# Optimization experiments

Measured on AMD Instinct MI355X. Metric: run time of the kernel, lower is better.

Reference implementation:

```python
import jax, jax.numpy as jnp
import numpy as np

# param tuples: (vdecay, vth, grad_win(=threshold_adaptation), grad_amp, rate_scale)
HID = (0.5, 0.3, 0.3, 1.0, 1.0)
OUT = (0.5, 0.3, 0.3, 1.0, 1.0)

B, I, H, O, T = 128, 1024, 4096, 512, 100


def setup_inputs() -> dict:
    key = jax.random.key(0)
    k1, k2, k3 = jax.random.split(key, 3)
    return {
        "spike_data": jax.random.uniform(k1, (B, I, T), dtype=jnp.float32),
        "hid_spike0": jnp.zeros((B, H), jnp.float32),
        "hid_volt0": jnp.zeros((B, H), jnp.float32),
        "out_spike0": jnp.zeros((B, O), jnp.float32),
        "out_volt0": jnp.zeros((B, O), jnp.float32),
        "w_hid": jax.random.normal(k2, (H, I), dtype=jnp.float32) * 0.02,
        "w_out": jax.random.normal(k3, (O, H), dtype=jnp.float32) * 0.02,
        "batch_size": B,
        "spike_ts": T,
    }


def _spike(volt, p):
    vdecay, vth, grad_win, grad_amp, rate_scale = p
    scaled = rate_scale * volt
    dyn_vth = vth * jnp.tanh(grad_win * jnp.max(scaled))
    return (scaled > dyn_vth).astype(volt.dtype)


def reference(spike_data, hid_spike0, hid_volt0, out_spike0, out_volt0,
              w_hid, w_out, batch_size, spike_ts):
    x = jnp.transpose(spike_data.reshape(batch_size, I, spike_ts), (2, 0, 1))  # [T,B,I]

    def step(carry, xt):
        hs, hv, osp, ov = carry
        hv_new = hv * HID[0] * (1.0 - hs) + xt @ w_hid.T          # [B,H]
        hs_new = _spike(hv_new, HID)
        ov_new = ov * OUT[0] * (1.0 - osp) + hs_new @ w_out.T     # [B,O]
        os_new = _spike(ov_new, OUT)
        return (hs_new, hv_new, os_new, ov_new), os_new

    _, outs = jax.lax.scan(step, (hid_spike0, hid_volt0, out_spike0, out_volt0), x)
    return jnp.sum(outs, axis=0)  # [B,O]
```

## Files before the change

### kernel.cpp

```cpp
#include <hip/hip_runtime.h>
#include <math.h>
#include <stdint.h>

#define T_STEPS 100
#define B_DIM 128
#define I_DIM 1024
#define H_DIM 4096
#define O_DIM 512
#define T_CHUNK 20
#define HS_RING 21
#define HS_SLOT ((size_t)8*128*512)
#define OV_LAG 21
#define RING_S 40
#define TAIL_START 80
#define LEADER 255

typedef _Float16 f16x8 __attribute__((ext_vector_type(8)));
typedef _Float16 f16x4 __attribute__((ext_vector_type(4)));
typedef float    f32x4 __attribute__((ext_vector_type(4)));

#define AS1 __attribute__((address_space(1)))
#define AS3 __attribute__((address_space(3)))

#define ALOAD(p)    __hip_atomic_load((p), __ATOMIC_RELAXED, __HIP_MEMORY_SCOPE_AGENT)
#define ASTORE(p,v) __hip_atomic_store((p), (v), __ATOMIC_RELAXED, __HIP_MEMORY_SCOPE_AGENT)

__device__ __forceinline__ void gload_lds16(const _Float16* g, _Float16* l){
  __builtin_amdgcn_global_load_lds(
      (const AS1 unsigned*)(uintptr_t)g,
      (AS3 unsigned*)(unsigned)(uintptr_t)l, 16, 0, 0);
}

__device__ __forceinline__ unsigned fmap(float f){
  unsigned u = __float_as_uint(f);
  return (u & 0x80000000u) ? ~u : (u | 0x80000000u);
}
__device__ __forceinline__ float funmap(unsigned m){
  unsigned u = (m & 0x80000000u) ? (m & 0x7FFFFFFFu) : ~m;
  return __uint_as_float(u);
}
__device__ __forceinline__ float vth_of(unsigned m){
  return 0.3f * tanhf(0.3f * funmap(m));
}

__global__ __launch_bounds__(256) void init_kernel(float* hv, float* ovs,
                                                   uint32_t* cnt32,
                                                   unsigned* hmaxA, unsigned* omaxA,
                                                   unsigned* hflag, unsigned* oflag)
{
  int i = blockIdx.x * 256 + threadIdx.x;
  if (i < B_DIM*H_DIM) hv[i] = 0.f;
  if (i < B_DIM*O_DIM) ovs[i] = 0.f;
  if (i < B_DIM*O_DIM/4) cnt32[i] = 0u;
  if (i < 100*256) hflag[i] = 0u;
  if (i < 101*32)  oflag[i] = 0u;
  if (i < 128){
    unsigned v = (i==0) ? 0x80000000u : 0u;
    hmaxA[i] = v; omaxA[i] = v;
  }
}

__global__ __launch_bounds__(256) void prep_x(const float* __restrict__ sp,
                                              _Float16* __restrict__ Ahi,
                                              _Float16* __restrict__ Alo, int t0)
{
  __shared__ float tile[32][16][10];
  const int b16 = blockIdx.x, kc = blockIdx.y, tz = blockIdx.z;
  for (int e = threadIdx.x; e < 5120; e += 256){
    int tt = e % 10, row = e / 10;
    int bb = row >> 5, ii = row & 31;
    tile[ii][bb][tt] =
      sp[((size_t)(b16*16+bb)*I_DIM + kc*32 + ii)*T_STEPS + t0 + tz*10 + tt];
  }
  __syncthreads();
  for (int u = threadIdx.x; u < 640; u += 256){
    int tl = u >> 6, l = u & 63, kg = l >> 4, r = l & 15;
    f16x8 hi, lo;
    #pragma unroll
    for (int e=0;e<8;e++){
      float x = tile[kg*8+e][r][tl] * 2048.f;
      _Float16 h = (_Float16)x;
      hi[e] = h;
      lo[e] = (_Float16)(x - (float)h);
    }
    int t_local = tz*10 + tl;
    size_t off = ((size_t)(t_local*8 + b16)*32 + kc)*512 + kg*128 + r*8;
    *(f16x8*)(Ahi + off) = hi;
    *(f16x8*)(Alo + off) = lo;
  }
}

__global__ __launch_bounds__(256) void prep_weights(
    const float* __restrict__ Wh, const float* __restrict__ Wo,
    _Float16* __restrict__ WHhi, _Float16* __restrict__ WHlo,
    _Float16* __restrict__ WOhi, _Float16* __restrict__ WOlo)
{
  const int blk = blockIdx.x;
  if (blk < 256){
    const int n16 = blk;
    for (int u = threadIdx.x; u < 2048; u += 256){
      int kc = u >> 6, l = u & 63, kg = l >> 4, r = l & 15;
      const float* src = Wh + (size_t)(n16*16 + r)*I_DIM + kc*32 + kg*8;
      f16x8 hi, lo;
      #pragma unroll
      for (int e=0;e<8;e++){
        float x = src[e] * 256.f;
        _Float16 h = (_Float16)x;
        hi[e] = h; lo[e] = (_Float16)(x - (float)h);
      }
      size_t off = ((size_t)n16*32 + kc)*512 + kg*128 + r*8;
      *(f16x8*)(WHhi + off) = hi;
      *(f16x8*)(WHlo + off) = lo;
    }
  } else {
    const int n16 = blk - 256;
    for (int u = threadIdx.x; u < 8192; u += 256){
      int kc = u >> 6, l = u & 63, kg = l >> 4, r = l & 15;
      const float* src = Wo + (size_t)(n16*16 + r)*H_DIM + kc*32 + kg*8;
      f16x8 hi, lo;
      #pragma unroll
      for (int e=0;e<8;e++){
        float x = src[e] * 256.f;
        _Float16 h = (_Float16)x;
        hi[e] = h; lo[e] = (_Float16)(x - (float)h);
      }
      size_t off = ((size_t)(n16*128 + kc))*512 + kg*128 + r*8;
      *(f16x8*)(WOhi + off) = hi;
      *(f16x8*)(WOlo + off) = lo;
    }
  }
}

__global__ __launch_bounds__(256, 2) void gemm1_mfma(
    const _Float16* __restrict__ Ahi, const _Float16* __restrict__ Alo,
    const _Float16* __restrict__ Bhi, const _Float16* __restrict__ Blo,
    float* __restrict__ G)
{
  __shared__ __align__(16) _Float16 lds[2][4][8][512];
  const int tid = threadIdx.x, wave = tid>>6, lane = tid&63;
  const int bn = blockIdx.x, bm = blockIdx.y;
  const int wm = wave>>1, wn = wave&1;

  const _Float16* srcbase = (wave==0)?Ahi:(wave==1)?Alo:(wave==2)?Bhi:Blo;
  const int r16b = ((wave<2) ? bm : bn)*8;
  const _Float16* gsrc = srcbase + (size_t)r16b*32*512 + lane*8;

  f32x4 acc[16];
  #pragma unroll
  for (int i=0;i<16;i++) acc[i] = (f32x4){0.f,0.f,0.f,0.f};

  #pragma unroll
  for (int q=0;q<8;q++)
    gload_lds16(gsrc + (size_t)q*32*512, &lds[0][wave][q][0]);

  for (int kc=0;kc<32;kc++){
    __syncthreads();
    if (kc < 31){
      #pragma unroll
      for (int q=0;q<8;q++)
        gload_lds16(gsrc + ((size_t)q*32 + kc+1)*512, &lds[(kc+1)&1][wave][q][0]);
    }
    const int cb = kc&1;
    f16x8 fAh[4], fAl[4], fBh[4], fBl[4];
    #pragma unroll
    for (int i=0;i<4;i++){
      fAh[i] = *(const f16x8*)&lds[cb][0][wm*4+i][lane*8];
      fAl[i] = *(const f16x8*)&lds[cb][1][wm*4+i][lane*8];
      fBh[i] = *(const f16x8*)&lds[cb][2][wn*4+i][lane*8];
      fBl[i] = *(const f16x8*)&lds[cb][3][wn*4+i][lane*8];
    }
    #pragma unroll
    for (int i=0;i<4;i++)
      #pragma unroll
      for (int j=0;j<4;j++)
        acc[i*4+j] = __builtin_amdgcn_mfma_f32_16x16x32_f16(fAh[i], fBh[j], acc[i*4+j], 0,0,0);
    #pragma unroll
    for (int i=0;i<4;i++)
      #pragma unroll
      for (int j=0;j<4;j++)
        acc[i*4+j] = __builtin_amdgcn_mfma_f32_16x16x32_f16(fAh[i], fBl[j], acc[i*4+j], 0,0,0);
    #pragma unroll
    for (int i=0;i<4;i++)
      #pragma unroll
      for (int j=0;j<4;j++)
        acc[i*4+j] = __builtin_amdgcn_mfma_f32_16x16x32_f16(fAl[i], fBh[j], acc[i*4+j], 0,0,0);
  }
  const int colw = lane&15, quad = lane>>4;
  const float sc = 1.f/(2048.f*256.f);
  float* eds = (float*)lds + wave*2048;
  __syncthreads();
  #pragma unroll
  for (int ih=0; ih<2; ih++){
    #pragma unroll
    for (int il=0; il<2; il++){
      int i = ih*2+il;
      #pragma unroll
      for (int j=0;j<4;j++)
        #pragma unroll
        for (int r=0;r<4;r++)
          eds[(il*16 + quad*4 + r)*64 + j*16 + colw] = acc[i*4+j][r]*sc;
    }
    #pragma unroll
    for (int rr8=0; rr8<8; rr8++){
      int row = rr8*4 + quad;
      float4 v = *(float4*)&eds[row*64 + colw*4];
      int m = bm*128 + wm*64 + ih*32 + row;
      int n = bn*128 + wn*64 + colw*4;
      *(float4*)&G[(size_t)m*H_DIM + n] = v;
    }
  }
}

__global__ __launch_bounds__(256) void hv_step(
    const float* __restrict__ Gs, float* __restrict__ hv,
    _Float16* __restrict__ hs_slot,
    const unsigned* __restrict__ hmax_t, unsigned* __restrict__ hmax_n, int t,
    const float* __restrict__ OGp, float* __restrict__ ovs,
    uchar4* __restrict__ cnt8, unsigned* __restrict__ omaxA, int ovt)
{
  __shared__ float red[4];
  const int tid = threadIdx.x, lane = tid&63, wv = tid>>6;

  if (blockIdx.x < 512){
    if (t > T_STEPS) return;
    const int gid = blockIdx.x*256 + tid;
    const int b = gid >> 10, h0 = (gid & 1023) << 2;
    const float vth = vth_of(*hmax_t);
    float4 h = *(const float4*)(hv + (size_t)gid*4);

    if (t > 0){
      const int kc = h0>>5, kg=(h0>>3)&3, e=h0&7, r=b&15, m16l=b>>4;
      f16x4 s;
      s[0]=(h.x>vth)?(_Float16)1:(_Float16)0; s[1]=(h.y>vth)?(_Float16)1:(_Float16)0;
      s[2]=(h.z>vth)?(_Float16)1:(_Float16)0; s[3]=(h.w>vth)?(_Float16)1:(_Float16)0;
      *(f16x4*)(hs_slot + ((size_t)m16l*128 + kc)*512 + kg*128 + r*8 + e) = s;
    }
    if (t < T_STEPS){
      float4 g = *(const float4*)(Gs + (size_t)gid*4);
      float4 o;
      o.x = (h.x>vth ? 0.f : 0.5f*h.x) + g.x;
      o.y = (h.y>vth ? 0.f : 0.5f*h.y) + g.y;
      o.z = (h.z>vth ? 0.f : 0.5f*h.z) + g.z;
      o.w = (h.w>vth ? 0.f : 0.5f*h.w) + g.w;
      *(float4*)(hv + (size_t)gid*4) = o;
      float lmax = fmaxf(fmaxf(o.x,o.y),fmaxf(o.z,o.w));
      #pragma unroll
      for (int off=32; off>0; off>>=1) lmax = fmaxf(lmax, __shfl_down(lmax, off));
      if (lane==0) red[wv] = lmax;
      __syncthreads();
      if (tid==0){
        float m = fmaxf(fmaxf(red[0],red[1]),fmaxf(red[2],red[3]));
        atomicMax(hmax_n, fmap(m));
      }
    }
  } else {
    if (ovt < 0 || ovt >= TAIL_START) return;
    const int f = (int)(blockIdx.x - 512)*256 + tid;
    const float vthp = vth_of(omaxA[ovt]);
    const int slot = ovt % RING_S;
    float lmax = -3.0e38f;
    #pragma unroll
    for (int q=0;q<4;q++){
      int o4 = f + q*4096;
      float4 v = *(const float4*)(ovs + (size_t)o4*4);
      uchar4 c = cnt8[o4];
      bool s0 = v.x > vthp, s1 = v.y > vthp, s2 = v.z > vthp, s3 = v.w > vthp;
      c.x += s0; c.y += s1; c.z += s2; c.w += s3;
      v.x = s0 ? 0.f : 0.5f*v.x;
      v.y = s1 ? 0.f : 0.5f*v.y;
      v.z = s2 ? 0.f : 0.5f*v.z;
      v.w = s3 ? 0.f : 0.5f*v.w;
      float4 g0 = *(const float4*)(OGp + ((size_t)slot*4+0)*(B_DIM*O_DIM) + (size_t)o4*4);
      float4 g1 = *(const float4*)(OGp + ((size_t)slot*4+1)*(B_DIM*O_DIM) + (size_t)o4*4);
      float4 g2 = *(const float4*)(OGp + ((size_t)slot*4+2)*(B_DIM*O_DIM) + (size_t)o4*4);
      float4 g3 = *(const float4*)(OGp + ((size_t)slot*4+3)*(B_DIM*O_DIM) + (size_t)o4*4);
      v.x += (g0.x+g1.x)+(g2.x+g3.x);
      v.y += (g0.y+g1.y)+(g2.y+g3.y);
      v.z += (g0.z+g1.z)+(g2.z+g3.z);
      v.w += (g0.w+g1.w)+(g2.w+g3.w);
      lmax = fmaxf(lmax, fmaxf(fmaxf(v.x,v.y),fmaxf(v.z,v.w)));
      *(float4*)(ovs + (size_t)o4*4) = v;
      cnt8[o4] = c;
    }
    #pragma unroll
    for (int off=32; off>0; off>>=1) lmax = fmaxf(lmax, __shfl_down(lmax, off));
    if (lane==0) red[wv] = lmax;
    __syncthreads();
    if (tid==0){
      float m = fmaxf(fmaxf(red[0],red[1]),fmaxf(red[2],red[3]));
      atomicMax(&omaxA[ovt+1], fmap(m));
    }
  }
}

__global__ __launch_bounds__(512) void hv_chunk(
    const float* __restrict__ Gs,
    float* __restrict__ hv,
    _Float16* __restrict__ HS,
    unsigned* __restrict__ hmaxA,
    const float* __restrict__ OGp, float* __restrict__ ovs,
    uchar4* __restrict__ cnt8, unsigned* __restrict__ omaxA,
    unsigned* __restrict__ hflag, unsigned* __restrict__ oflag,
    int t0, int nsteps)
{
  __shared__ float red[8], redo[8];
  __shared__ unsigned sredH[4];
  __shared__ unsigned sh_h, sh_o;
  const int tid = threadIdx.x, lane = tid&63, wv = tid>>6;
  const int blk = blockIdx.x;
  const int gid = blk*512 + tid;
  const int b = gid >> 10, h0 = (gid & 1023) << 2;
  const int kc = h0>>5, kg=(h0>>3)&3, e=h0&7, r=b&15, m16l=b>>4;
  const bool ovblk = blk < 32;

  float4 h = *(const float4*)(hv + (size_t)gid*4);
  float4 vo = make_float4(0.f,0.f,0.f,0.f);
  unsigned cw = 0;
  if (ovblk){
    vo = *(const float4*)(ovs + (size_t)gid*4);
    uchar4 c0 = cnt8[gid];
    cw = (unsigned)c0.x | ((unsigned)c0.y<<8) | ((unsigned)c0.z<<16) | ((unsigned)c0.w<<24);
  }
  float4 g = *(const float4*)(Gs + (size_t)gid*4);
  unsigned hm_cur = hmaxA[t0];
  unsigned om_cur = 0;
  { int ovt0 = t0 - OV_LAG;
    if (ovblk && ovt0 >= 0 && ovt0 < TAIL_START) om_cur = omaxA[ovt0]; }

  for (int j = 0; j < nsteps; j++){
    const int t = t0 + j;
    const int ovt = t - OV_LAG;
    const bool last = (j == nsteps-1);

    float4 gn = make_float4(0.f,0.f,0.f,0.f);
    if (!last && (t+1) < T_STEPS)
      gn = *(const float4*)(Gs + (size_t)(j+1)*(B_DIM*H_DIM) + (size_t)gid*4);

    const float vth = vth_of(hm_cur);
    {
      f16x4 s;
      s[0]=(h.x>vth)?(_Float16)1:(_Float16)0; s[1]=(h.y>vth)?(_Float16)1:(_Float16)0;
      s[2]=(h.z>vth)?(_Float16)1:(_Float16)0; s[3]=(h.w>vth)?(_Float16)1:(_Float16)0;
      _Float16* slotp = HS + (size_t)((t-1)%HS_RING)*HS_SLOT;
      *(f16x4*)(slotp + ((size_t)m16l*128 + kc)*512 + kg*128 + r*8 + e) = s;
    }
    float lmax = -3.0e38f;
    if (t < T_STEPS){
      h.x = (h.x>vth ? 0.f : 0.5f*h.x) + g.x;
      h.y = (h.y>vth ? 0.f : 0.5f*h.y) + g.y;
      h.z = (h.z>vth ? 0.f : 0.5f*h.z) + g.z;
      h.w = (h.w>vth ? 0.f : 0.5f*h.w) + g.w;
      lmax = fmaxf(fmaxf(h.x,h.y),fmaxf(h.z,h.w));
    }

    const bool rid = ovblk && ovt >= 0 && ovt < TAIL_START;
    float omax_l = -3.0e38f;
    if (rid){
      const float vthp = vth_of(om_cur);
      const int slot = ovt % RING_S;
      bool s0 = vo.x > vthp, s1 = vo.y > vthp, s2 = vo.z > vthp, s3 = vo.w > vthp;
      cw += (s0?1u:0u) | (s1?(1u<<8):0u) | (s2?(1u<<16):0u) | (s3?(1u<<24):0u);
      vo.x = s0 ? 0.f : 0.5f*vo.x;
      vo.y = s1 ? 0.f : 0.5f*vo.y;
      vo.z = s2 ? 0.f : 0.5f*vo.z;
      vo.w = s3 ? 0.f : 0.5f*vo.w;
      float4 g0 = *(const float4*)(OGp + ((size_t)slot*4+0)*(B_DIM*O_DIM) + (size_t)gid*4);
      float4 g1 = *(const float4*)(OGp + ((size_t)slot*4+1)*(B_DIM*O_DIM) + (size_t)gid*4);
      float4 g2 = *(const float4*)(OGp + ((size_t)slot*4+2)*(B_DIM*O_DIM) + (size_t)gid*4);
      float4 g3 = *(const float4*)(OGp + ((size_t)slot*4+3)*(B_DIM*O_DIM) + (size_t)gid*4);
      vo.x += (g0.x+g1.x)+(g2.x+g3.x);
      vo.y += (g0.y+g1.y)+(g2.y+g3.y);
      vo.z += (g0.z+g1.z)+(g2.z+g3.z);
      vo.w += (g0.w+g1.w)+(g2.w+g3.w);
      omax_l = fmaxf(fmaxf(vo.x,vo.y),fmaxf(vo.z,vo.w));
    }

    #pragma unroll
    for (int off2=32; off2>0; off2>>=1) lmax = fmaxf(lmax, __shfl_down(lmax, off2));
    if (lane==0) red[wv] = lmax;
    if (ovblk){
      #pragma unroll
      for (int off2=32; off2>0; off2>>=1) omax_l = fmaxf(omax_l, __shfl_down(omax_l, off2));
      if (lane==0) redo[wv] = omax_l;
    }
    __syncthreads();

    if (tid == 0 && t < T_STEPS){
      float m = red[0];
      #pragma unroll
      for (int w2=1; w2<8; w2++) m = fmaxf(m, red[w2]);
      ASTORE(&hflag[(size_t)t*256 + blk], fmap(m));
    }
    if (tid == 0 && rid){
      float mo = redo[0];
      #pragma unroll
      for (int w2=1; w2<8; w2++) mo = fmaxf(mo, redo[w2]);
      ASTORE(&oflag[(size_t)ovt*32 + blk], fmap(mo));
    }

    if (blk == LEADER){
      if (t < T_STEPS && tid < 256){
        unsigned v;
        while (!(v = ALOAD(&hflag[(size_t)t*256 + tid])))
          __builtin_amdgcn_s_sleep(1);
        #pragma unroll
        for (int off2=32; off2>0; off2>>=1){
          unsigned o = (unsigned)__shfl_down((int)v, off2);
          if (o > v) v = o;
        }
        if (lane==0) sredH[wv] = v;
      }
      if (tid >= 256 && tid < 320){
        unsigned v = 0;
        if (tid < 288 && ovt >= 0 && ovt < TAIL_START){
          while (!(v = ALOAD(&oflag[(size_t)ovt*32 + (tid-256)])))
            __builtin_amdgcn_s_sleep(1);
        }
        #pragma unroll
        for (int off2=32; off2>0; off2>>=1){
          unsigned o = (unsigned)__shfl_down((int)v, off2);
          if (o > v) v = o;
        }
        if (tid == 256 && ovt >= 0 && ovt < TAIL_START)
          ASTORE(&omaxA[ovt+1], v);
      }
      __syncthreads();
      if (tid == 0 && t < T_STEPS){
        unsigned m = sredH[0];
        if (sredH[1] > m) m = sredH[1];
        if (sredH[2] > m) m = sredH[2];
        if (sredH[3] > m) m = sredH[3];
        ASTORE(&hmaxA[t+1], m);
      }
    }

    if (!last){
      if (tid == 0){
        unsigned v;
        while (!(v = ALOAD(&hmaxA[t+1])))
          __builtin_amdgcn_s_sleep(1);
        sh_h = v;
        if (ovblk && (ovt+1) >= 0 && (ovt+1) < TAIL_START){
          unsigned v2;
          while (!(v2 = ALOAD(&omaxA[ovt+1])))
            __builtin_amdgcn_s_sleep(1);
          sh_o = v2;
        }
      }
      __syncthreads();
      hm_cur = sh_h;
      if (ovblk) om_cur = sh_o;
      g = gn;
    }
  }

  *(float4*)(hv + (size_t)gid*4) = h;
  if (ovblk){
    *(float4*)(ovs + (size_t)gid*4) = vo;
    cnt8[gid] = make_uchar4((unsigned char)(cw & 0xffu),
                            (unsigned char)((cw>>8) & 0xffu),
                            (unsigned char)((cw>>16) & 0xffu),
                            (unsigned char)((cw>>24) & 0xffu));
  }
}

__global__ __launch_bounds__(256, 2) void gemm2_mfma(
    const _Float16* __restrict__ HS,
    const _Float16* __restrict__ WoHi, const _Float16* __restrict__ WoLo,
    float* __restrict__ OGp, int c)
{
  __shared__ __align__(16) _Float16 lds2[2][24][512];
  const int tid = threadIdx.x, wave = tid>>6, lane = tid&63;
  const int bn = blockIdx.x, bm = blockIdx.y, kh = blockIdx.z;
  const int s = c*T_CHUNK + bm, ring = s % HS_RING;
  const int wm = wave>>1, wn = wave&1;
  const int kc0 = kh*32;

  const _Float16* baseA = HS   + (size_t)ring*8*128*512 + lane*8;
  const _Float16* baseH = WoHi + (size_t)bn*8*128*512 + lane*8;
  const _Float16* baseL = WoLo + (size_t)bn*8*128*512 + lane*8;

  f32x4 acc[16];
  #pragma unroll
  for (int i=0;i<16;i++) acc[i] = (f32x4){0.f,0.f,0.f,0.f};

  #pragma unroll
  for (int i=0;i<6;i++){
    int f = wave*6 + i;
    const _Float16* g = (f<8)  ? baseA + ((size_t)f*128      + kc0)*512
                     : (f<16) ? baseH + ((size_t)(f-8)*128  + kc0)*512
                              : baseL + ((size_t)(f-16)*128 + kc0)*512;
    gload_lds16(g, &lds2[0][f][0]);
  }

  for (int k=0;k<32;k++){
    __syncthreads();
    if (k < 31){
      #pragma unroll
      for (int i=0;i<6;i++){
        int f = wave*6 + i;
        const _Float16* g = (f<8)  ? baseA + ((size_t)f*128      + kc0+k+1)*512
                         : (f<16) ? baseH + ((size_t)(f-8)*128  + kc0+k+1)*512
                                  : baseL + ((size_t)(f-16)*128 + kc0+k+1)*512;
        gload_lds16(g, &lds2[(k+1)&1][f][0]);
      }
    }
    const int cb = k&1;
    f16x8 fA[4], fH[4], fL[4];
    #pragma unroll
    for (int i=0;i<4;i++){
      fA[i] = *(const f16x8*)&lds2[cb][wm*4+i][lane*8];
      fH[i] = *(const f16x8*)&lds2[cb][8+wn*4+i][lane*8];
      fL[i] = *(const f16x8*)&lds2[cb][16+wn*4+i][lane*8];
    }
    #pragma unroll
    for (int i=0;i<4;i++)
      #pragma unroll
      for (int j=0;j<4;j++)
        acc[i*4+j] = __builtin_amdgcn_mfma_f32_16x16x32_f16(fA[i], fH[j], acc[i*4+j], 0,0,0);
    #pragma unroll
    for (int i=0;i<4;i++)
      #pragma unroll
      for (int j=0;j<4;j++)
        acc[i*4+j] = __builtin_amdgcn_mfma_f32_16x16x32_f16(fA[i], fL[j], acc[i*4+j], 0,0,0);
  }
  const int colw = lane&15, quad = lane>>4;
  const float sc = 1.f/256.f;
  float* eds = (float*)lds2 + wave*2048;
  __syncthreads();
  float* OGd = OGp + ((size_t)(s % RING_S)*4 + kh)*(B_DIM*O_DIM);
  #pragma unroll
  for (int ih=0; ih<2; ih++){
    #pragma unroll
    for (int il=0; il<2; il++){
      int i = ih*2+il;
      #pragma unroll
      for (int j=0;j<4;j++)
        #pragma unroll
        for (int r=0;r<4;r++)
          eds[(il*16 + quad*4 + r)*64 + j*16 + colw] = acc[i*4+j][r]*sc;
    }
    #pragma unroll
    for (int rr8=0; rr8<8; rr8++){
      int row = rr8*4 + quad;
      float4 v = *(float4*)&eds[row*64 + colw*4];
      int m = wm*64 + ih*32 + row;
      int n = bn*128 + wn*64 + colw*4;
      *(float4*)&OGd[(size_t)m*O_DIM + n] = v;
    }
  }
}

__global__ __launch_bounds__(256) void ov_tail(
    const float* __restrict__ OGp, const float* __restrict__ ovs,
    const uchar4* __restrict__ cnt8, unsigned* __restrict__ omaxA,
    unsigned* __restrict__ oflag, float* __restrict__ out)
{
  __shared__ float red[4];
  __shared__ unsigned sh_o;
  const int tid = threadIdx.x, lane = tid&63, wv = tid>>6;
  const int f = blockIdx.x*256 + tid;
  float ov[16];
  unsigned cw[4];
  #pragma unroll
  for (int q=0;q<4;q++){
    int o4 = f + q*4096;
    float4 v = *(const float4*)(ovs + (size_t)o4*4);
    ov[q*4+0]=v.x; ov[q*4+1]=v.y; ov[q*4+2]=v.z; ov[q*4+3]=v.w;
    uchar4 c = cnt8[o4];
    cw[q] = (unsigned)c.x | ((unsigned)c.y<<8) | ((unsigned)c.z<<16) | ((unsigned)c.w<<24);
  }
  unsigned om_cur = omaxA[TAIL_START];

  for (int ovt = TAIL_START; ovt <= T_STEPS; ovt++){
    const float vth = vth_of(om_cur);
    const int slot = ovt % RING_S;
    float lmax = -3.0e38f;
    #pragma unroll
    for (int q=0;q<4;q++){
      int o4 = f + q*4096;
      #pragma unroll
      for (int e=0;e<4;e++){
        int idx = q*4+e;
        bool os = ov[idx] > vth;
        cw[q] += os ? (1u<<(e*8)) : 0u;
        ov[idx] = os ? 0.f : 0.5f*ov[idx];
      }
      if (ovt < T_STEPS){
        float4 g0 = *(const float4*)(OGp + ((size_t)slot*4+0)*(B_DIM*O_DIM) + (size_t)o4*4);
        float4 g1 = *(const float4*)(OGp + ((size_t)slot*4+1)*(B_DIM*O_DIM) + (size_t)o4*4);
        float4 g2 = *(const float4*)(OGp + ((size_t)slot*4+2)*(B_DIM*O_DIM) + (size_t)o4*4);
        float4 g3 = *(const float4*)(OGp + ((size_t)slot*4+3)*(B_DIM*O_DIM) + (size_t)o4*4);
        ov[q*4+0] += (g0.x+g1.x)+(g2.x+g3.x);
        ov[q*4+1] += (g0.y+g1.y)+(g2.y+g3.y);
        ov[q*4+2] += (g0.z+g1.z)+(g2.z+g3.z);
        ov[q*4+3] += (g0.w+g1.w)+(g2.w+g3.w);
        lmax = fmaxf(lmax, fmaxf(fmaxf(ov[q*4+0],ov[q*4+1]),fmaxf(ov[q*4+2],ov[q*4+3])));
      }
    }
    if (ovt == T_STEPS) break;
    #pragma unroll
    for (int off=32; off>0; off>>=1) lmax = fmaxf(lmax, __shfl_down(lmax, off));
    if (lane==0) red[wv] = lmax;
    __syncthreads();
    if (tid==0){
      float m = fmaxf(fmaxf(red[0],red[1]),fmaxf(red[2],red[3]));
      ASTORE(&oflag[(size_t)ovt*32 + blockIdx.x], fmap(m));
    }
    if (blockIdx.x == 0 && tid < 64){
      unsigned v = 0;
      if (tid < 16){
        while (!(v = ALOAD(&oflag[(size_t)ovt*32 + tid])))
          __builtin_amdgcn_s_sleep(1);
      }
      #pragma unroll
      for (int off=32; off>0; off>>=1){
        unsigned o = (unsigned)__shfl_down((int)v, off);
        if (o > v) v = o;
      }
      if (tid == 0) ASTORE(&omaxA[ovt+1], v);
    }
    if (tid==0){
      unsigned v;
      while (!(v = ALOAD(&omaxA[ovt+1])))
        __builtin_amdgcn_s_sleep(1);
      sh_o = v;
    }
    __syncthreads();
    om_cur = sh_o;
  }
  #pragma unroll
  for (int q=0;q<4;q++){
    int o4 = f + q*4096;
    *(float4*)(out + (size_t)o4*4) = make_float4(
        (float)( cw[q]        & 0xffu),
        (float)((cw[q] >> 8)  & 0xffu),
        (float)((cw[q] >> 16) & 0xffu),
        (float)((cw[q] >> 24) & 0xffu));
  }
}

extern "C" void kernel_launch(void* const* d_in, const int* in_sizes, int n_in,
                              void* d_out, int out_size, void* d_ws, size_t ws_size,
                              hipStream_t stream) {
  const float* spike = (const float*)d_in[0];
  const float* Wh    = (const float*)d_in[5];
  const float* Wo    = (const float*)d_in[6];
  float* out = (float*)d_out;

  char* ws = (char*)d_ws;
  size_t off = 0;
  _Float16* XAhi = (_Float16*)(ws+off); off += (size_t)T_CHUNK*B_DIM*I_DIM*2;
  _Float16* XAlo = (_Float16*)(ws+off); off += (size_t)T_CHUNK*B_DIM*I_DIM*2;
  _Float16* WHhi = (_Float16*)(ws+off); off += (size_t)H_DIM*I_DIM*2;
  _Float16* WHlo = (_Float16*)(ws+off); off += (size_t)H_DIM*I_DIM*2;
  _Float16* WOhi = (_Float16*)(ws+off); off += (size_t)O_DIM*H_DIM*2;
  _Float16* WOlo = (_Float16*)(ws+off); off += (size_t)O_DIM*H_DIM*2;
  float* G  = (float*)(ws+off);         off += (size_t)T_CHUNK*B_DIM*H_DIM*4;
  float* hv = (float*)(ws+off);         off += (size_t)B_DIM*H_DIM*4;
  _Float16* HS = (_Float16*)(ws+off);   off += (size_t)HS_RING*HS_SLOT*2;
  float* OGp = (float*)(ws+off);        off += (size_t)RING_S*4*B_DIM*O_DIM*4;
  float* ovs = (float*)(ws+off);        off += (size_t)B_DIM*O_DIM*4;
  uchar4* cnt8 = (uchar4*)(ws+off);     off += (size_t)B_DIM*O_DIM;
  unsigned* hmaxA = (unsigned*)(ws+off); off += 128*4;
  unsigned* omaxA = (unsigned*)(ws+off); off += 128*4;
  unsigned* hflag = (unsigned*)(ws+off); off += (size_t)100*256*4;
  unsigned* oflag = (unsigned*)(ws+off); off += (size_t)101*32*4;
  (void)ws_size; (void)in_sizes; (void)n_in; (void)out_size;

  init_kernel<<<(B_DIM*H_DIM+255)/256, 256, 0, stream>>>(
      hv, ovs, (uint32_t*)cnt8, hmaxA, omaxA, hflag, oflag);
  prep_weights<<<288, 256, 0, stream>>>(Wh, Wo, WHhi, WHlo, WOhi, WOlo);

  for (int c = 0; c < T_STEPS/T_CHUNK; c++){
    prep_x<<<dim3(8,32,2), 256, 0, stream>>>(spike, XAhi, XAlo, c*T_CHUNK);
    gemm1_mfma<<<dim3(32, T_CHUNK), 256, 0, stream>>>(XAhi, XAlo, WHhi, WHlo, G);
    {
      int t = c*T_CHUNK;
      int ring = (t == 0) ? (HS_RING-1) : ((t-1) % HS_RING);
      hv_step<<<528, 256, 0, stream>>>(
          G, hv, HS + (size_t)ring*HS_SLOT,
          hmaxA + t, hmaxA + t + 1, t,
          OGp, ovs, cnt8, omaxA, t - OV_LAG);
    }
    if (c > 0)
      gemm2_mfma<<<dim3(4, T_CHUNK, 4), 256, 0, stream>>>(HS, WOhi, WOlo, OGp, c-1);
    {
      int nsteps = (c == T_STEPS/T_CHUNK - 1) ? T_CHUNK : (T_CHUNK - 1);
      hv_chunk<<<256, 512, 0, stream>>>(
          G + (size_t)B_DIM*H_DIM, hv, HS, hmaxA,
          OGp, ovs, cnt8, omaxA, hflag, oflag,
          c*T_CHUNK + 1, nsteps);
    }
  }
  gemm2_mfma<<<dim3(4, T_CHUNK, 4), 256, 0, stream>>>(HS, WOhi, WOlo, OGp, T_STEPS/T_CHUNK - 1);
  ov_tail<<<16, 256, 0, stream>>>(OGp, ovs, cnt8, omaxA, oflag, out);
}
```

Measured before the change: 1.127 ms.

## Replace leader-broadcast grid barrier with all-block flag polling and prefetch OG slices

In hv_chunk, every block now polls the per-block max flags itself with 64-bit paired atomic loads and reduces them locally. This replaces the old scheme where a leader block reduced the flags and the others then waited on its broadcast, so one global round trip is removed from each step's grid synchronisation. The output-gradient slices for the next step are loaded one step ahead in hv_chunk and in ov_tail. ov_tail is respread over 128 blocks of 128 threads with a decentralised flag barrier. The catch is heavier polling traffic, because every block spins on the same flag lines.

```diff
diff --git a/kernel.cpp b/kernel.cpp
--- a/kernel.cpp
+++ b/kernel.cpp
@@ -43,10 +43,30 @@
   return 0.3f * tanhf(0.3f * funmap(m));
 }
 
+__device__ __forceinline__ unsigned poll2max(const unsigned* base, int idx){
+  const unsigned long long* p = (const unsigned long long*)base + idx;
+  unsigned long long v = ALOAD(p);
+  while (((unsigned)v) == 0u || ((unsigned)(v >> 32)) == 0u){
+    __builtin_amdgcn_s_sleep(1);
+    v = ALOAD(p);
+  }
+  unsigned lo = (unsigned)v, hi = (unsigned)(v >> 32);
+  return lo > hi ? lo : hi;
+}
+__device__ __forceinline__ unsigned wred_umax(unsigned v){
+  #pragma unroll
+  for (int o = 32; o > 0; o >>= 1){
+    unsigned t = (unsigned)__shfl_down((int)v, o);
+    if (t > v) v = t;
+  }
+  return v;
+}
+
 __global__ __launch_bounds__(256) void init_kernel(float* hv, float* ovs,
                                                    uint32_t* cnt32,
                                                    unsigned* hmaxA, unsigned* omaxA,
-                                                   unsigned* hflag, unsigned* oflag)
+                                                   unsigned* hflag, unsigned* oflag,
+                                                   unsigned* otflag)
 {
   int i = blockIdx.x * 256 + threadIdx.x;
   if (i < B_DIM*H_DIM) hv[i] = 0.f;
@@ -54,6 +74,7 @@
   if (i < B_DIM*O_DIM/4) cnt32[i] = 0u;
   if (i < 100*256) hflag[i] = 0u;
   if (i < 101*32)  oflag[i] = 0u;
+  if (i < 20*128)  otflag[i] = 0u;
   if (i < 128){
     unsigned v = (i==0) ? 0x80000000u : 0u;
     hmaxA[i] = v; omaxA[i] = v;
@@ -304,14 +325,16 @@
     int t0, int nsteps)
 {
   __shared__ float red[8], redo[8];
-  __shared__ unsigned sredH[4];
-  __shared__ unsigned sh_h, sh_o;
+  __shared__ unsigned sredH[2];
+  __shared__ unsigned sredO;
   const int tid = threadIdx.x, lane = tid&63, wv = tid>>6;
   const int blk = blockIdx.x;
   const int gid = blk*512 + tid;
   const int b = gid >> 10, h0 = (gid & 1023) << 2;
   const int kc = h0>>5, kg=(h0>>3)&3, e=h0&7, r=b&15, m16l=b>>4;
   const bool ovblk = blk < 32;
+  const int ovt0 = t0 - OV_LAG;
+  const bool rid = ovblk && (ovt0 >= 0);
 
   float4 h = *(const float4*)(hv + (size_t)gid*4);
   float4 vo = make_float4(0.f,0.f,0.f,0.f);
@@ -323,9 +346,18 @@
   }
   float4 g = *(const float4*)(Gs + (size_t)gid*4);
   unsigned hm_cur = hmaxA[t0];
-  unsigned om_cur = 0;
-  { int ovt0 = t0 - OV_LAG;
-    if (ovblk && ovt0 >= 0 && ovt0 < TAIL_START) om_cur = omaxA[ovt0]; }
+  unsigned om_cur = rid ? omaxA[ovt0] : 0;
+
+  float4 og0,og1,og2,og3;
+  og0=og1=og2=og3=make_float4(0.f,0.f,0.f,0.f);
+  if (rid){
+    const int sl = ovt0 % RING_S;
+    const float* base = OGp + (size_t)gid*4;
+    og0 = *(const float4*)(base + (size_t)(sl*4+0)*(B_DIM*O_DIM));
+    og1 = *(const float4*)(base + (size_t)(sl*4+1)*(B_DIM*O_DIM));
+    og2 = *(const float4*)(base + (size_t)(sl*4+2)*(B_DIM*O_DIM));
+    og3 = *(const float4*)(base + (size_t)(sl*4+3)*(B_DIM*O_DIM));
+  }
 
   for (int j = 0; j < nsteps; j++){
     const int t = t0 + j;
@@ -335,6 +367,16 @@
     float4 gn = make_float4(0.f,0.f,0.f,0.f);
     if (!last && (t+1) < T_STEPS)
       gn = *(const float4*)(Gs + (size_t)(j+1)*(B_DIM*H_DIM) + (size_t)gid*4);
+    float4 on0,on1,on2,on3;
+    on0=on1=on2=on3=make_float4(0.f,0.f,0.f,0.f);
+    if (rid && !last){
+      const int sln = (ovt+1) % RING_S;
+      const float* base = OGp + (size_t)gid*4;
+      on0 = *(const float4*)(base + (size_t)(sln*4+0)*(B_DIM*O_DIM));
+      on1 = *(const float4*)(base + (size_t)(sln*4+1)*(B_DIM*O_DIM));
+      on2 = *(const float4*)(base + (size_t)(sln*4+2)*(B_DIM*O_DIM));
+      on3 = *(const float4*)(base + (size_t)(sln*4+3)*(B_DIM*O_DIM));
+    }
 
     const float vth = vth_of(hm_cur);
     {
@@ -353,32 +395,26 @@
       lmax = fmaxf(fmaxf(h.x,h.y),fmaxf(h.z,h.w));
     }
 
-    const bool rid = ovblk && ovt >= 0 && ovt < TAIL_START;
     float omax_l = -3.0e38f;
     if (rid){
       const float vthp = vth_of(om_cur);
-      const int slot = ovt % RING_S;
       bool s0 = vo.x > vthp, s1 = vo.y > vthp, s2 = vo.z > vthp, s3 = vo.w > vthp;
       cw += (s0?1u:0u) | (s1?(1u<<8):0u) | (s2?(1u<<16):0u) | (s3?(1u<<24):0u);
       vo.x = s0 ? 0.f : 0.5f*vo.x;
       vo.y = s1 ? 0.f : 0.5f*vo.y;
       vo.z = s2 ? 0.f : 0.5f*vo.z;
       vo.w = s3 ? 0.f : 0.5f*vo.w;
-      float4 g0 = *(const float4*)(OGp + ((size_t)slot*4+0)*(B_DIM*O_DIM) + (size_t)gid*4);
-      float4 g1 = *(const float4*)(OGp + ((size_t)slot*4+1)*(B_DIM*O_DIM) + (size_t)gid*4);
-      float4 g2 = *(const float4*)(OGp + ((size_t)slot*4+2)*(B_DIM*O_DIM) + (size_t)gid*4);
-      float4 g3 = *(const float4*)(OGp + ((size_t)slot*4+3)*(B_DIM*O_DIM) + (size_t)gid*4);
-      vo.x += (g0.x+g1.x)+(g2.x+g3.x);
-      vo.y += (g0.y+g1.y)+(g2.y+g3.y);
-      vo.z += (g0.z+g1.z)+(g2.z+g3.z);
-      vo.w += (g0.w+g1.w)+(g2.w+g3.w);
+      vo.x += (og0.x+og1.x)+(og2.x+og3.x);
+      vo.y += (og0.y+og1.y)+(og2.y+og3.y);
+      vo.z += (og0.z+og1.z)+(og2.z+og3.z);
+      vo.w += (og0.w+og1.w)+(og2.w+og3.w);
       omax_l = fmaxf(fmaxf(vo.x,vo.y),fmaxf(vo.z,vo.w));
     }
 
     #pragma unroll
     for (int off2=32; off2>0; off2>>=1) lmax = fmaxf(lmax, __shfl_down(lmax, off2));
     if (lane==0) red[wv] = lmax;
-    if (ovblk){
+    if (rid){
       #pragma unroll
       for (int off2=32; off2>0; off2>>=1) omax_l = fmaxf(omax_l, __shfl_down(omax_l, off2));
       if (lane==0) redo[wv] = omax_l;
@@ -398,59 +434,47 @@
       ASTORE(&oflag[(size_t)ovt*32 + blk], fmap(mo));
     }
 
-    if (blk == LEADER){
-      if (t < T_STEPS && tid < 256){
-        unsigned v;
-        while (!(v = ALOAD(&hflag[(size_t)t*256 + tid])))
-          __builtin_amdgcn_s_sleep(1);
-        #pragma unroll
-        for (int off2=32; off2>0; off2>>=1){
-          unsigned o = (unsigned)__shfl_down((int)v, off2);
-          if (o > v) v = o;
-        }
-        if (lane==0) sredH[wv] = v;
+    if (!last){
+      if (tid < 128){
+        unsigned mx = poll2max(hflag + (size_t)t*256, tid);
+        mx = wred_umax(mx);
+        if (lane == 0) sredH[wv] = mx;
       }
-      if (tid >= 256 && tid < 320){
-        unsigned v = 0;
-        if (tid < 288 && ovt >= 0 && ovt < TAIL_START){
-          while (!(v = ALOAD(&oflag[(size_t)ovt*32 + (tid-256)])))
-            __builtin_amdgcn_s_sleep(1);
-        }
-        #pragma unroll
-        for (int off2=32; off2>0; off2>>=1){
-          unsigned o = (unsigned)__shfl_down((int)v, off2);
-          if (o > v) v = o;
-        }
-        if (tid == 256 && ovt >= 0 && ovt < TAIL_START)
-          ASTORE(&omaxA[ovt+1], v);
+      if (rid && tid >= 128 && tid < 192){
+        unsigned mx = 0;
+        if (tid < 144) mx = poll2max(oflag + (size_t)ovt*32, tid - 128);
+        mx = wred_umax(mx);
+        if (lane == 0) sredO = mx;
       }
       __syncthreads();
-      if (tid == 0 && t < T_STEPS){
-        unsigned m = sredH[0];
-        if (sredH[1] > m) m = sredH[1];
-        if (sredH[2] > m) m = sredH[2];
-        if (sredH[3] > m) m = sredH[3];
-        ASTORE(&hmaxA[t+1], m);
-      }
-    }
-
-    if (!last){
-      if (tid == 0){
-        unsigned v;
-        while (!(v = ALOAD(&hmaxA[t+1])))
-          __builtin_amdgcn_s_sleep(1);
-        sh_h = v;
-        if (ovblk && (ovt+1) >= 0 && (ovt+1) < TAIL_START){
-          unsigned v2;
-          while (!(v2 = ALOAD(&omaxA[ovt+1])))
-            __builtin_amdgcn_s_sleep(1);
-          sh_o = v2;
+      { unsigned m0 = sredH[0], m1 = sredH[1];
+        hm_cur = m0 > m1 ? m0 : m1; }
+      if (rid) om_cur = sredO;
+      if (blk == LEADER && tid == 0) ASTORE(&hmaxA[t+1], hm_cur);
+      if (blk == 0 && rid && tid == 0) ASTORE(&omaxA[ovt+1], om_cur);
+      g = gn;
+      og0=on0; og1=on1; og2=on2; og3=on3;
+    } else {
+      if (blk == LEADER && t < T_STEPS){
+        if (tid < 128){
+          unsigned mx = poll2max(hflag + (size_t)t*256, tid);
+          mx = wred_umax(mx);
+          if (lane == 0) sredH[wv] = mx;
+        }
+        __syncthreads();
+        if (tid == 0){
+          unsigned m0 = sredH[0], m1 = sredH[1];
+          ASTORE(&hmaxA[t+1], m0 > m1 ? m0 : m1);
         }
       }
-      __syncthreads();
-      hm_cur = sh_h;
-      if (ovblk) om_cur = sh_o;
-      g = gn;
+      if (blk == 0 && rid){
+        if (tid < 64){
+          unsigned mx = 0;
+          if (tid < 16) mx = poll2max(oflag + (size_t)ovt*32, tid);
+          mx = wred_umax(mx);
+          if (tid == 0) ASTORE(&omaxA[ovt+1], mx);
+        }
+      }
     }
   }
 
@@ -551,93 +575,75 @@
   }
 }
 
-__global__ __launch_bounds__(256) void ov_tail(
+__global__ __launch_bounds__(128) void ov_tail(
     const float* __restrict__ OGp, const float* __restrict__ ovs,
-    const uchar4* __restrict__ cnt8, unsigned* __restrict__ omaxA,
-    unsigned* __restrict__ oflag, float* __restrict__ out)
+    const uchar4* __restrict__ cnt8, const unsigned* __restrict__ omaxA,
+    unsigned* __restrict__ otflag, float* __restrict__ out)
 {
-  __shared__ float red[4];
-  __shared__ unsigned sh_o;
+  __shared__ float red[2];
+  __shared__ unsigned shm;
   const int tid = threadIdx.x, lane = tid&63, wv = tid>>6;
-  const int f = blockIdx.x*256 + tid;
-  float ov[16];
-  unsigned cw[4];
-  #pragma unroll
-  for (int q=0;q<4;q++){
-    int o4 = f + q*4096;
-    float4 v = *(const float4*)(ovs + (size_t)o4*4);
-    ov[q*4+0]=v.x; ov[q*4+1]=v.y; ov[q*4+2]=v.z; ov[q*4+3]=v.w;
-    uchar4 c = cnt8[o4];
-    cw[q] = (unsigned)c.x | ((unsigned)c.y<<8) | ((unsigned)c.z<<16) | ((unsigned)c.w<<24);
-  }
+  const int f = blockIdx.x*128 + tid;
+  float4 ov = *(const float4*)(ovs + (size_t)f*4);
+  uchar4 c0 = cnt8[f];
+  unsigned cw = (unsigned)c0.x | ((unsigned)c0.y<<8) | ((unsigned)c0.z<<16) | ((unsigned)c0.w<<24);
   unsigned om_cur = omaxA[TAIL_START];
 
+  float4 og0,og1,og2,og3;
+  {
+    const int sl = TAIL_START % RING_S;
+    const float* base = OGp + (size_t)f*4;
+    og0 = *(const float4*)(base + (size_t)(sl*4+0)*(B_DIM*O_DIM));
+    og1 = *(const float4*)(base + (size_t)(sl*4+1)*(B_DIM*O_DIM));
+    og2 = *(const float4*)(base + (size_t)(sl*4+2)*(B_DIM*O_DIM));
+    og3 = *(const float4*)(base + (size_t)(sl*4+3)*(B_DIM*O_DIM));
+  }
+
   for (int ovt = TAIL_START; ovt <= T_STEPS; ovt++){
+    float4 n0,n1,n2,n3;
+    n0=n1=n2=n3=make_float4(0.f,0.f,0.f,0.f);
+    if ((ovt+1) < T_STEPS){
+      const int sl = (ovt+1) % RING_S;
+      const float* base = OGp + (size_t)f*4;
+      n0 = *(const float4*)(base + (size_t)(sl*4+0)*(B_DIM*O_DIM));
+      n1 = *(const float4*)(base + (size_t)(sl*4+1)*(B_DIM*O_DIM));
+      n2 = *(const float4*)(base + (size_t)(sl*4+2)*(B_DIM*O_DIM));
+      n3 = *(const float4*)(base + (size_t)(sl*4+3)*(B_DIM*O_DIM));
+    }
     const float vth = vth_of(om_cur);
-    const int slot = ovt % RING_S;
-    float lmax = -3.0e38f;
-    #pragma unroll
-    for (int q=0;q<4;q++){
-      int o4 = f + q*4096;
-      #pragma unroll
-      for (int e=0;e<4;e++){
-        int idx = q*4+e;
-        bool os = ov[idx] > vth;
-        cw[q] += os ? (1u<<(e*8)) : 0u;
-        ov[idx] = os ? 0.f : 0.5f*ov[idx];
-      }
-      if (ovt < T_STEPS){
-        float4 g0 = *(const float4*)(OGp + ((size_t)slot*4+0)*(B_DIM*O_DIM) + (size_t)o4*4);
-        float4 g1 = *(const float4*)(OGp + ((size_t)slot*4+1)*(B_DIM*O_DIM) + (size_t)o4*4);
-        float4 g2 = *(const float4*)(OGp + ((size_t)slot*4+2)*(B_DIM*O_DIM) + (size_t)o4*4);
-        float4 g3 = *(const float4*)(OGp + ((size_t)slot*4+3)*(B_DIM*O_DIM) + (size_t)o4*4);
-        ov[q*4+0] += (g0.x+g1.x)+(g2.x+g3.x);
-        ov[q*4+1] += (g0.y+g1.y)+(g2.y+g3.y);
-        ov[q*4+2] += (g0.z+g1.z)+(g2.z+g3.z);
-        ov[q*4+3] += (g0.w+g1.w)+(g2.w+g3.w);
-        lmax = fmaxf(lmax, fmaxf(fmaxf(ov[q*4+0],ov[q*4+1]),fmaxf(ov[q*4+2],ov[q*4+3])));
-      }
-    }
+    bool s0 = ov.x > vth, s1 = ov.y > vth, s2 = ov.z > vth, s3 = ov.w > vth;
+    cw += (s0?1u:0u) | (s1?(1u<<8):0u) | (s2?(1u<<16):0u) | (s3?(1u<<24):0u);
+    ov.x = s0 ? 0.f : 0.5f*ov.x;
+    ov.y = s1 ? 0.f : 0.5f*ov.y;
+    ov.z = s2 ? 0.f : 0.5f*ov.z;
+    ov.w = s3 ? 0.f : 0.5f*ov.w;
     if (ovt == T_STEPS) break;
+    ov.x += (og0.x+og1.x)+(og2.x+og3.x);
+    ov.y += (og0.y+og1.y)+(og2.y+og3.y);
+    ov.z += (og0.z+og1.z)+(og2.z+og3.z);
+    ov.w += (og0.w+og1.w)+(og2.w+og3.w);
+    float lmax = fmaxf(fmaxf(ov.x,ov.y),fmaxf(ov.z,ov.w));
     #pragma unroll
     for (int off=32; off>0; off>>=1) lmax = fmaxf(lmax, __shfl_down(lmax, off));
     if (lane==0) red[wv] = lmax;
     __syncthreads();
-    if (tid==0){
-      float m = fmaxf(fmaxf(red[0],red[1]),fmaxf(red[2],red[3]));
-      ASTORE(&oflag[(size_t)ovt*32 + blockIdx.x], fmap(m));
-    }
-    if (blockIdx.x == 0 && tid < 64){
-      unsigned v = 0;
-      if (tid < 16){
-        while (!(v = ALOAD(&oflag[(size_t)ovt*32 + tid])))
-          __builtin_amdgcn_s_sleep(1);
-      }
-      #pragma unroll
-      for (int off=32; off>0; off>>=1){
-        unsigned o = (unsigned)__shfl_down((int)v, off);
-        if (o > v) v = o;
-      }
-      if (tid == 0) ASTORE(&omaxA[ovt+1], v);
-    }
-    if (tid==0){
-      unsigned v;
-      while (!(v = ALOAD(&omaxA[ovt+1])))
-        __builtin_amdgcn_s_sleep(1);
-      sh_o = v;
+    if (tid==0)
+      ASTORE(&otflag[(size_t)(ovt-TAIL_START)*128 + blockIdx.x],
+             fmap(fmaxf(red[0], red[1])));
+    if (tid < 64){
+      unsigned mx = poll2max(otflag + (size_t)(ovt-TAIL_START)*128, tid);
+      mx = wred_umax(mx);
+      if (tid == 0) shm = mx;
     }
     __syncthreads();
-    om_cur = sh_o;
-  }
-  #pragma unroll
-  for (int q=0;q<4;q++){
-    int o4 = f + q*4096;
-    *(float4*)(out + (size_t)o4*4) = make_float4(
-        (float)( cw[q]        & 0xffu),
-        (float)((cw[q] >> 8)  & 0xffu),
-        (float)((cw[q] >> 16) & 0xffu),
-        (float)((cw[q] >> 24) & 0xffu));
-  }
+    om_cur = shm;
+    og0=n0; og1=n1; og2=n2; og3=n3;
+  }
+  *(float4*)(out + (size_t)f*4) = make_float4(
+      (float)( cw        & 0xffu),
+      (float)((cw >> 8)  & 0xffu),
+      (float)((cw >> 16) & 0xffu),
+      (float)((cw >> 24) & 0xffu));
 }
 
 extern "C" void kernel_launch(void* const* d_in, const int* in_sizes, int n_in,
@@ -666,10 +672,11 @@
   unsigned* omaxA = (unsigned*)(ws+off); off += 128*4;
   unsigned* hflag = (unsigned*)(ws+off); off += (size_t)100*256*4;
   unsigned* oflag = (unsigned*)(ws+off); off += (size_t)101*32*4;
+  unsigned* otflag = (unsigned*)(ws+off); off += (size_t)20*128*4;
   (void)ws_size; (void)in_sizes; (void)n_in; (void)out_size;
 
   init_kernel<<<(B_DIM*H_DIM+255)/256, 256, 0, stream>>>(
-      hv, ovs, (uint32_t*)cnt8, hmaxA, omaxA, hflag, oflag);
+      hv, ovs, (uint32_t*)cnt8, hmaxA, omaxA, hflag, oflag, otflag);
   prep_weights<<<288, 256, 0, stream>>>(Wh, Wo, WHhi, WHlo, WOhi, WOlo);
 
   for (int c = 0; c < T_STEPS/T_CHUNK; c++){
@@ -694,5 +701,5 @@
     }
   }
   gemm2_mfma<<<dim3(4, T_CHUNK, 4), 256, 0, stream>>>(HS, WOhi, WOlo, OGp, T_STEPS/T_CHUNK - 1);
-  ov_tail<<<16, 256, 0, stream>>>(OGp, ovs, cnt8, omaxA, oflag, out);
-}
+  ov_tail<<<128, 128, 0, stream>>>(OGp, ovs, cnt8, omaxA, otflag, out);
+}
```

After: 1.236 ms. 9.7% more time.
